# Kernel optimization log

Measured on AMD Instinct MI355X. Metric: run time of the kernel, lower is better.

## Reference

```python
import jax, jax.numpy as jnp
import numpy as np

VOCAB = 50000; T = 4096; EMBED = 500; H = 500  # hidden per direction (HIDDEN_SIZE=1000, bidirectional)
NUM_TAGS = 16; START = 14; STOP = 15
NEG = -10000.0


def setup_inputs() -> dict:
    key = jax.random.key(0)
    ks = jax.random.split(key, 16)
    n = lambda k, s, sc=0.1: (jax.random.normal(k, s) * sc).astype(jnp.float32)
    trans = n(ks[12], (NUM_TAGS, NUM_TAGS), 1.0)
    trans = trans.at[START, :].set(NEG).at[:, STOP].set(NEG)  # as in __init__
    return {
        "sent": jax.random.randint(ks[0], (T,), 0, VOCAB),
        "embed_w": n(ks[1], (VOCAB, EMBED), 1.0),
        "wih0": n(ks[2], (2, 4 * H, EMBED)),
        "whh0": n(ks[3], (2, 4 * H, H)),
        "bih0": n(ks[4], (2, 4 * H)),
        "bhh0": n(ks[5], (2, 4 * H)),
        "wih1": n(ks[6], (2, 4 * H, 2 * H)),
        "whh1": n(ks[7], (2, 4 * H, H)),
        "bih1": n(ks[8], (2, 4 * H)),
        "bhh1": n(ks[9], (2, 4 * H)),
        "w_out": n(ks[10], (NUM_TAGS, 2 * H)),
        "b_out": n(ks[11], (NUM_TAGS,)),
        "trans": trans,
        "h0": n(ks[13], (4, H), 1.0),  # init_hidden() uses randn; layout [layer*2+dir, H]
        "c0": n(ks[14], (4, H), 1.0),
    }


def _lstm_dir(x, wih, whh, bih, bhh, h0, c0):
    b = bih + bhh
    def cell(carry, xt):
        h, c = carry
        g = xt @ wih.T + h @ whh.T + b          # [4H], torch gate order i,f,g,o
        i, f, gg, o = jnp.split(g, 4)
        c = jax.nn.sigmoid(f) * c + jax.nn.sigmoid(i) * jnp.tanh(gg)
        h = jax.nn.sigmoid(o) * jnp.tanh(c)
        return (h, c), h
    _, hs = jax.lax.scan(cell, (h0, c0), x)
    return hs  # [T, H]


def _bilstm_layer(x, wih, whh, bih, bhh, h0, c0):
    fwd = _lstm_dir(x, wih[0], whh[0], bih[0], bhh[0], h0[0], c0[0])
    bwd = _lstm_dir(x[::-1], wih[1], whh[1], bih[1], bhh[1], h0[1], c0[1])[::-1]
    return jnp.concatenate([fwd, bwd], axis=-1)  # [T, 2H]


def _features(sent, embed_w, wih0, whh0, bih0, bhh0, wih1, whh1, bih1, bhh1, w_out, b_out, h0, c0):
    x = embed_w[sent]                                            # [T, EMBED]
    x = _bilstm_layer(x, wih0, whh0, bih0, bhh0, h0[0:2], c0[0:2])
    x = _bilstm_layer(x, wih1, whh1, bih1, bhh1, h0[2:4], c0[2:4])
    return x @ w_out.T + b_out                                   # [T, NUM_TAGS]


def _viterbi(feats, trans):
    score0 = jnp.full((NUM_TAGS,), NEG, dtype=feats.dtype).at[START].set(0.0)
    def step(score, feat):
        m = score[None, :] + trans               # m[tag, prev] = score[prev] + trans[tag, prev]
        return jnp.max(m, axis=1) + feat, jnp.argmax(m, axis=1)
    score, bptr = jax.lax.scan(step, score0, feats)              # bptr: [T, NUM_TAGS]
    score = score + trans[STOP]
    best_tag = jnp.argmax(score)
    best_score = score[best_tag]
    # faithful to the source backtrace: best_tag is NOT updated inside its loop,
    # so path = [bptr[1][bt], ..., bptr[T-1][bt], bt]
    path = jnp.concatenate([bptr[1:, best_tag], best_tag[None]])
    return best_score, path


def reference(sent, embed_w, wih0, whh0, bih0, bhh0, wih1, whh1, bih1, bhh1, w_out, b_out, trans, h0, c0):
    feats = _features(sent, embed_w, wih0, whh0, bih0, bhh0,
                      wih1, whh1, bih1, bhh1, w_out, b_out, h0, c0)
    return _viterbi(feats, trans)
```

## Files before the change

### kernel.cpp

```cpp
#include <hip/hip_runtime.h>


#define T_SEQ 4096
#define HPAD  512
#define NTAG  16


__global__ __launch_bounds__(256) void gin_gemm_k(
    const float* __restrict__ A, int KA,
    const int* __restrict__ sent, const float* __restrict__ embed_w,
    const float* __restrict__ wih, const float* __restrict__ bih,
    const float* __restrict__ bhh, int Kreal, float* __restrict__ G) {
  const int dir = blockIdx.z;
  const int bm = blockIdx.y, bn = blockIdx.x;
  const float* W = wih + (size_t)dir * 2000 * Kreal;

  __shared__ float As[2][16][128];
  __shared__ float Bs[2][16][128];
  __shared__ int   sSent[128];

  const int tid = threadIdx.x;
  const int tx = tid & 15, ty = tid >> 4;

  if (sent && tid < 128) sSent[tid] = sent[bm * 128 + tid];
  if (sent) __syncthreads();

  const int mA[2] = { (tid + 0) >> 2, (tid + 256) >> 2 };
  const int kA[2] = { ((tid + 0) & 3) * 4, ((tid + 256) & 3) * 4 };

  auto loadA = [&](int k0, int q) -> float4 {
    int m = mA[q], kc = kA[q];
    int k = k0 + kc;
    if (sent) {
      float4 z = {0.f, 0.f, 0.f, 0.f};
      if (k < 500)
        z = *reinterpret_cast<const float4*>(&embed_w[(size_t)sSent[m] * 500 + k]);
      return z;
    }
    return *reinterpret_cast<const float4*>(&A[(size_t)(bm * 128 + m) * KA + k]);
  };
  auto loadB = [&](int k0, int q) -> float4 {
    int n = mA[q], kc = kA[q];
    int nn = bn * 128 + n;
    int gate = nn >> 9, j = nn & 511;
    int k = k0 + kc;
    int jk = k & 511, half = k >> 9;
    float4 z = {0.f, 0.f, 0.f, 0.f};
    if (j < 500 && jk < 500)
      z = *reinterpret_cast<const float4*>(
          &W[(size_t)(gate * 500 + j) * Kreal + half * 500 + jk]);
    return z;
  };
  auto store = [&](int buf, int q, float4 av, float4 bv) {
    int m = mA[q], kc = kA[q];
    As[buf][kc + 0][m] = av.x; As[buf][kc + 1][m] = av.y;
    As[buf][kc + 2][m] = av.z; As[buf][kc + 3][m] = av.w;
    Bs[buf][kc + 0][m] = bv.x; Bs[buf][kc + 1][m] = bv.y;
    Bs[buf][kc + 2][m] = bv.z; Bs[buf][kc + 3][m] = bv.w;
  };

  {
    float4 a0 = loadA(0, 0), b0 = loadB(0, 0);
    float4 a1 = loadA(0, 1), b1 = loadB(0, 1);
    store(0, 0, a0, b0);
    store(0, 1, a1, b1);
  }
  __syncthreads();

  const int iters = KA >> 4;
  float acc[8][8] = {};

  for (int it = 0; it < iters; ++it) {
    const int cur = it & 1;
    const bool hasNext = (it + 1 < iters);
    float4 aP0, bP0, aP1, bP1;
    if (hasNext) {
      int k0n = (it + 1) << 4;
      aP0 = loadA(k0n, 0); bP0 = loadB(k0n, 0);
      aP1 = loadA(k0n, 1); bP1 = loadB(k0n, 1);
    }
#pragma unroll
    for (int kk = 0; kk < 16; kk++) {
      float a[8], b[8];
      *reinterpret_cast<float4*>(&a[0]) = *reinterpret_cast<const float4*>(&As[cur][kk][ty * 8]);
      *reinterpret_cast<float4*>(&a[4]) = *reinterpret_cast<const float4*>(&As[cur][kk][ty * 8 + 4]);
      *reinterpret_cast<float4*>(&b[0]) = *reinterpret_cast<const float4*>(&Bs[cur][kk][tx * 8]);
      *reinterpret_cast<float4*>(&b[4]) = *reinterpret_cast<const float4*>(&Bs[cur][kk][tx * 8 + 4]);
#pragma unroll
      for (int i = 0; i < 8; i++)
#pragma unroll
        for (int j = 0; j < 8; j++) acc[i][j] = fmaf(a[i], b[j], acc[i][j]);
    }
    if (hasNext) {
      store(cur ^ 1, 0, aP0, bP0);
      store(cur ^ 1, 1, aP1, bP1);
    }
    __syncthreads();
  }

#pragma unroll
  for (int i = 0; i < 8; i++) {
#pragma unroll
    for (int j = 0; j < 8; j++) {
      int m = bm * 128 + ty * 8 + i;
      int nn = bn * 128 + tx * 8 + j;
      int gate = nn >> 9, ju = nn & 511;
      float o = 0.0f;
      if (ju < 500) {
        int r = gate * 500 + ju;
        o = acc[i][j] + bih[dir * 2000 + r] + bhh[dir * 2000 + r];
      }
      G[((size_t)dir * T_SEQ + m) * 2048 + nn] = o;
    }
  }
}

__device__ __forceinline__ unsigned long long pack_hv(unsigned tag, float h) {
  return (unsigned long long)tag | ((unsigned long long)__float_as_uint(h) << 32);
}

__device__ __forceinline__ float fsig(float x) {
  float e = __expf(-x);
  return __builtin_amdgcn_rcpf(1.0f + e);
}
__device__ __forceinline__ float ftanhf(float x) {
  return fmaf(2.0f, fsig(x + x), -1.0f);
}

__global__ void hinit_k(const float* __restrict__ h0, int layer,
                        unsigned long long* __restrict__ hcomm) {
  int i = blockIdx.x * blockDim.x + threadIdx.x;
  int dir = i >> 10, par = (i >> 9) & 1, j = i & 511;
  unsigned long long v;
  if (par == 0) {
    float h = (j < 500) ? h0[(layer * 2 + dir) * 500 + j] : 0.0f;
    v = pack_hv(0u, h);
  } else {
    v = 0xFFFFFFFFull;
  }
  hcomm[(size_t)(dir * 2 + par) * HPAD + j] = v;
}

__global__ __launch_bounds__(1024)
__attribute__((amdgpu_waves_per_eu(4, 4)))
void lstm_k(
    const float* __restrict__ whh_base,
    const float* __restrict__ gin,
    const float* __restrict__ c0,
    float* __restrict__ xout,
    unsigned long long* __restrict__ hcomm,
    int layer) {
  __shared__ float part[16][68];
  __shared__ float hbuf[16][32];

  const int tid = threadIdx.x;
  const int dir = blockIdx.x >> 5;
  const int wgd = blockIdx.x & 31;
  const int w = tid >> 6;
  const int lane = tid & 63;

  const int gate = lane >> 4;
  const int ul   = lane & 15;
  const int j    = wgd * 16 + ul;
  const int row  = gate * 500 + j;

  float wreg[32];
  const float* Wd = whh_base + (size_t)dir * 2000 * 500;
#pragma unroll
  for (int i = 0; i < 32; i++) {
    int k = w * 32 + i;
    wreg[i] = (j < 500 && k < 500) ? Wd[(size_t)row * 500 + k] : 0.0f;
  }
#pragma unroll
  for (int i = 0; i < 32; i++) asm volatile("" : "+v"(wreg[i]));

  float c = 0.0f;
  if (w == 0 && lane < 16 && j < 500) c = c0[(layer * 2 + dir) * 500 + j];

  unsigned long long* hcd = hcomm + (size_t)dir * 2 * HPAD;
  bool dead = false;

  for (int t = 0; t < T_SEQ; t++) {
    const int t_in = (dir == 0) ? t : (T_SEQ - 1 - t);

    float gi = 0.0f;
    if (w == 0) {
      const float* gb = gin + ((size_t)dir * T_SEQ + t_in) * 2048;
      gi = gb[gate * 512 + j];
    }

    unsigned long long v = 0;
    if (!dead) {
      const unsigned long long* hp =
          hcd + (size_t)(t & 1) * HPAD + w * 32 + (lane & 31);
      int guard = 0;
      for (;;) {
        v = __hip_atomic_load(hp, __ATOMIC_RELAXED, __HIP_MEMORY_SCOPE_AGENT);
        if (__all((int)((unsigned)v == (unsigned)t))) break;
        if (++guard > (1 << 22)) { dead = true; break; }
      }
    }
    float hval = __uint_as_float((unsigned)(v >> 32));

    if (lane < 32) hbuf[w][lane] = hval;
    float a = 0.0f;
#pragma unroll
    for (int b = 0; b < 8; b++) {
      float4 hv = *reinterpret_cast<const float4*>(&hbuf[w][b * 4]);
      a = fmaf(wreg[b * 4 + 0], hv.x, a);
      a = fmaf(wreg[b * 4 + 1], hv.y, a);
      a = fmaf(wreg[b * 4 + 2], hv.z, a);
      a = fmaf(wreg[b * 4 + 3], hv.w, a);
    }
    part[w][lane] = a;
    __syncthreads();

    if (w == 0) {
      __builtin_amdgcn_s_setprio(1);
      float p0 = part[0][lane] + part[1][lane];
      float p1 = part[2][lane] + part[3][lane];
      float p2 = part[4][lane] + part[5][lane];
      float p3 = part[6][lane] + part[7][lane];
      float p4 = part[8][lane] + part[9][lane];
      float p5 = part[10][lane] + part[11][lane];
      float p6 = part[12][lane] + part[13][lane];
      float p7 = part[14][lane] + part[15][lane];
      float q0 = p0 + p1, q1 = p2 + p3, q2 = p4 + p5, q3 = p6 + p7;
      float s = gi + ((q0 + q1) + (q2 + q3));
      float nl = (gate == 2) ? ftanhf(s) : fsig(s);
      float xf = __shfl(nl, lane + 16, 64);
      float xg = __shfl(nl, lane + 32, 64);
      float xo = __shfl(nl, lane + 48, 64);
      if (lane < 16) {
        c = xf * c + nl * xg;
        float h = xo * ftanhf(c);
        __hip_atomic_store(hcd + (size_t)((t + 1) & 1) * HPAD + j,
                           pack_hv((unsigned)(t + 1), h),
                           __ATOMIC_RELAXED, __HIP_MEMORY_SCOPE_AGENT);
        if (j < 500)
          xout[(size_t)t_in * 1024 + (size_t)dir * HPAD + j] = h;
      }
      __builtin_amdgcn_s_setprio(0);
    }
  }
}

__global__ __launch_bounds__(256) void feats_k(
    const float* __restrict__ x2, const float* __restrict__ w_out,
    const float* __restrict__ b_out, float* __restrict__ feats) {
  int tid = threadIdx.x;
  int tag = tid & 15, tl = tid >> 4;
  int t = blockIdx.x * 16 + tl;
  float a0 = 0.0f, a1 = 0.0f, a2 = 0.0f, a3 = 0.0f;
  for (int k = 0; k < 1024; k += 4) {
    int jk = k & 511;
    const float* xr = x2 + (size_t)t * 1024 + k;
    const float* wr = w_out + tag * 1000 + (k >> 9) * 500 + jk;
    if (jk + 3 < 500) {
      a0 = fmaf(xr[0], wr[0], a0);
      a1 = fmaf(xr[1], wr[1], a1);
      a2 = fmaf(xr[2], wr[2], a2);
      a3 = fmaf(xr[3], wr[3], a3);
    } else if (jk < 500) {
#pragma unroll
      for (int e = 0; e < 4; e++)
        if (jk + e < 500) a0 = fmaf(xr[e], wr[e], a0);
    }
  }
  feats[t * 16 + tag] = ((a0 + a1) + (a2 + a3)) + b_out[tag];
}

__global__ __launch_bounds__(64) void viterbi_k(
    const float* __restrict__ feats, const float* __restrict__ trans,
    int* __restrict__ bptr, float* __restrict__ out) {
  int tid = threadIdx.x;
  int tag = tid & 15, pg = tid >> 4;
  float tr0 = trans[tag * 16 + pg * 4 + 0];
  float tr1 = trans[tag * 16 + pg * 4 + 1];
  float tr2 = trans[tag * 16 + pg * 4 + 2];
  float tr3 = trans[tag * 16 + pg * 4 + 3];
  float s = (tag == 14) ? 0.0f : -10000.0f;
  float ft = feats[tag];
  for (int t = 0; t < T_SEQ; t++) {
    float ftn = (t + 1 < T_SEQ) ? feats[(t + 1) * 16 + tag] : 0.0f;
    float c0 = __shfl(s, pg * 4 + 0, 64) + tr0;
    float c1 = __shfl(s, pg * 4 + 1, 64) + tr1;
    float c2 = __shfl(s, pg * 4 + 2, 64) + tr2;
    float c3 = __shfl(s, pg * 4 + 3, 64) + tr3;
    float bv = c0; int bi = pg * 4;
    if (c1 > bv) { bv = c1; bi = pg * 4 + 1; }
    if (c2 > bv) { bv = c2; bi = pg * 4 + 2; }
    if (c3 > bv) { bv = c3; bi = pg * 4 + 3; }
    float ov = __shfl_xor(bv, 16, 64); int oi = __shfl_xor(bi, 16, 64);
    if (ov > bv || (ov == bv && oi < bi)) { bv = ov; bi = oi; }
    ov = __shfl_xor(bv, 32, 64); oi = __shfl_xor(bi, 32, 64);
    if (ov > bv || (ov == bv && oi < bi)) { bv = ov; bi = oi; }
    s = bv + ft;
    ft = ftn;
    if (pg == 0) bptr[t * 16 + tag] = bi;
  }
  s += trans[15 * 16 + tag];
  float bv = s; int bi = tag;
  for (int mask = 1; mask < 16; mask <<= 1) {
    float ov = __shfl_xor(bv, mask, 16); int oi = __shfl_xor(bi, mask, 16);
    if (ov > bv || (ov == bv && oi < bi)) { bv = ov; bi = oi; }
  }
  if (tid == 0) out[0] = bv;
  int bt = bi;
  for (int i = tid; i < T_SEQ - 1; i += 64)
    out[1 + i] = (float)bptr[(i + 1) * 16 + bt];
  if (tid == 0) out[T_SEQ] = (float)bt;
}

extern "C" void kernel_launch(void* const* d_in, const int* in_sizes, int n_in,
                              void* d_out, int out_size, void* d_ws, size_t ws_size,
                              hipStream_t stream) {
  const int*   sent  = (const int*)d_in[0];
  const float* embed = (const float*)d_in[1];
  const float* wih0  = (const float*)d_in[2];
  const float* whh0  = (const float*)d_in[3];
  const float* bih0  = (const float*)d_in[4];
  const float* bhh0  = (const float*)d_in[5];
  const float* wih1  = (const float*)d_in[6];
  const float* whh1  = (const float*)d_in[7];
  const float* bih1  = (const float*)d_in[8];
  const float* bhh1  = (const float*)d_in[9];
  const float* w_out = (const float*)d_in[10];
  const float* b_out = (const float*)d_in[11];
  const float* trans = (const float*)d_in[12];
  const float* h0    = (const float*)d_in[13];
  const float* c0    = (const float*)d_in[14];
  float* out = (float*)d_out;

  char* ws = (char*)d_ws;
  float* x1    = (float*)(ws + 8388608);
  float* x2    = (float*)(ws + 25165824);
  float* gin   = (float*)(ws + 41943040);
  float* feats = (float*)(ws + 109051904);
  int*   bptr  = (int*)(ws + 109314048);
  unsigned long long* hcomm = (unsigned long long*)(ws + 109576192);

  gin_gemm_k<<<dim3(16, 32, 2), 256, 0, stream>>>(nullptr, 512, sent, embed,
                                                  wih0, bih0, bhh0, 500, gin);
  hinit_k<<<2, 1024, 0, stream>>>(h0, 0, hcomm);
  lstm_k<<<64, 1024, 0, stream>>>(whh0, gin, c0, x1, hcomm, 0);

  gin_gemm_k<<<dim3(16, 32, 2), 256, 0, stream>>>(x1, 1024, nullptr, nullptr,
                                                  wih1, bih1, bhh1, 1000, gin);
  hinit_k<<<2, 1024, 0, stream>>>(h0, 1, hcomm);
  lstm_k<<<64, 1024, 0, stream>>>(whh1, gin, c0, x2, hcomm, 1);

  feats_k<<<T_SEQ / 16, 256, 0, stream>>>(x2, w_out, b_out, feats);
  viterbi_k<<<1, 64, 0, stream>>>(feats, trans, bptr, out);
}
```

Before: 13.16 ms.

## Overlap layer-1 input GEMM with layer-0 recurrence via persistent progress queue

Fuses the layer-0 LSTM recurrence and the layer-1 input-projection GEMM into one persistent kernel. Extra workgroups take GEMM tiles from an atomic ticket counter and spin on per-workgroup progress flags until both directions have produced the required rows of x1. Tiles are ordered from the middle of the sequence outward, where forward and backward outputs become complete first. This hides most of the second GEMM behind the serial recurrence. The cost is contention from the GEMM workgroups for CU resources and memory bandwidth, which could slow the latency-critical recurrence, and reliance on cross-workgroup spin-waits.

Result: slower. 23.94 ms (+81.9%).

```diff
diff --git a/kernel.cpp b/kernel.cpp
--- a/kernel.cpp
+++ b/kernel.cpp
@@ -128,8 +128,11 @@
 }
 
 __global__ void hinit_k(const float* __restrict__ h0, int layer,
-                        unsigned long long* __restrict__ hcomm) {
+                        unsigned long long* __restrict__ hcomm,
+                        int* __restrict__ progq) {
   int i = blockIdx.x * blockDim.x + threadIdx.x;
+  if (i < 64) progq[i] = -1;
+  if (i == 64) progq[64] = 0;
   int dir = i >> 10, par = (i >> 9) & 1, j = i & 511;
   unsigned long long v;
   if (par == 0) {
@@ -143,13 +146,207 @@
 
 __global__ __launch_bounds__(1024)
 __attribute__((amdgpu_waves_per_eu(4, 4)))
-void lstm_k(
+void lstm_gemm_k(
     const float* __restrict__ whh_base,
     const float* __restrict__ gin,
     const float* __restrict__ c0,
     float* __restrict__ xout,
     unsigned long long* __restrict__ hcomm,
-    int layer) {
+    int* __restrict__ progq,
+    const float* __restrict__ wih1,
+    const float* __restrict__ bih1, const float* __restrict__ bhh1) {
+  __shared__ float part[16][68];
+  __shared__ float hbuf[16][32];
+  __shared__ float wAs[16][256];
+  __shared__ float wBs[16][128];
+  __shared__ int sTicket;
+
+  const int tid = threadIdx.x;
+  float* ginw = (float*)gin;
+
+  if (blockIdx.x < 64) {
+    const int dir = blockIdx.x >> 5;
+    const int wgd = blockIdx.x & 31;
+    const int w = tid >> 6;
+    const int lane = tid & 63;
+
+    const int gate = lane >> 4;
+    const int ul   = lane & 15;
+    const int j    = wgd * 16 + ul;
+    const int row  = gate * 500 + j;
+
+    float wreg[32];
+    const float* Wd = whh_base + (size_t)dir * 2000 * 500;
+#pragma unroll
+    for (int i = 0; i < 32; i++) {
+      int k = w * 32 + i;
+      wreg[i] = (j < 500 && k < 500) ? Wd[(size_t)row * 500 + k] : 0.0f;
+    }
+#pragma unroll
+    for (int i = 0; i < 32; i++) asm volatile("" : "+v"(wreg[i]));
+
+    float c = 0.0f;
+    if (w == 0 && lane < 16 && j < 500) c = c0[(0 * 2 + dir) * 500 + j];
+
+    unsigned long long* hcd = hcomm + (size_t)dir * 2 * HPAD;
+    bool dead = false;
+
+    for (int t = 0; t < T_SEQ; t++) {
+      const int t_in = (dir == 0) ? t : (T_SEQ - 1 - t);
+
+      float gi = 0.0f;
+      if (w == 0) {
+        const float* gb = gin + ((size_t)dir * T_SEQ + t_in) * 2048;
+        gi = gb[gate * 512 + j];
+      }
+
+      unsigned long long v = 0;
+      if (!dead) {
+        const unsigned long long* hp =
+            hcd + (size_t)(t & 1) * HPAD + w * 32 + (lane & 31);
+        int guard = 0;
+        for (;;) {
+          v = __hip_atomic_load(hp, __ATOMIC_RELAXED, __HIP_MEMORY_SCOPE_AGENT);
+          if (__all((int)((unsigned)v == (unsigned)t))) break;
+          if (++guard > (1 << 22)) { dead = true; break; }
+        }
+      }
+      float hval = __uint_as_float((unsigned)(v >> 32));
+
+      if (lane < 32) hbuf[w][lane] = hval;
+      float a = 0.0f;
+#pragma unroll
+      for (int b = 0; b < 8; b++) {
+        float4 hv = *reinterpret_cast<const float4*>(&hbuf[w][b * 4]);
+        a = fmaf(wreg[b * 4 + 0], hv.x, a);
+        a = fmaf(wreg[b * 4 + 1], hv.y, a);
+        a = fmaf(wreg[b * 4 + 2], hv.z, a);
+        a = fmaf(wreg[b * 4 + 3], hv.w, a);
+      }
+      part[w][lane] = a;
+      __syncthreads();
+
+      if (w == 0) {
+        __builtin_amdgcn_s_setprio(1);
+        float p0 = part[0][lane] + part[1][lane];
+        float p1 = part[2][lane] + part[3][lane];
+        float p2 = part[4][lane] + part[5][lane];
+        float p3 = part[6][lane] + part[7][lane];
+        float p4 = part[8][lane] + part[9][lane];
+        float p5 = part[10][lane] + part[11][lane];
+        float p6 = part[12][lane] + part[13][lane];
+        float p7 = part[14][lane] + part[15][lane];
+        float q0 = p0 + p1, q1 = p2 + p3, q2 = p4 + p5, q3 = p6 + p7;
+        float s = gi + ((q0 + q1) + (q2 + q3));
+        float nl = (gate == 2) ? ftanhf(s) : fsig(s);
+        float xf = __shfl(nl, lane + 16, 64);
+        float xg = __shfl(nl, lane + 32, 64);
+        float xo = __shfl(nl, lane + 48, 64);
+        if (lane < 16) {
+          c = xf * c + nl * xg;
+          float h = xo * ftanhf(c);
+          __hip_atomic_store(hcd + (size_t)((t + 1) & 1) * HPAD + j,
+                             pack_hv((unsigned)(t + 1), h),
+                             __ATOMIC_RELAXED, __HIP_MEMORY_SCOPE_AGENT);
+          if (j < 500)
+            xout[(size_t)t_in * 1024 + (size_t)dir * HPAD + j] = h;
+          if (lane == 0 && (t & 31) == 31)
+            __hip_atomic_store(&progq[dir * 32 + wgd], t,
+                               __ATOMIC_RELEASE, __HIP_MEMORY_SCOPE_AGENT);
+        }
+        __builtin_amdgcn_s_setprio(0);
+      }
+    }
+    return;
+  }
+
+  const int ty = tid >> 4, tx = tid & 15;
+  for (;;) {
+    if (tid == 0) sTicket = atomicAdd(&progq[64], 1);
+    __syncthreads();
+    int q = sTicket;
+    __syncthreads();
+    if (q >= 512) break;
+    int r = q >> 5;
+    int bm = (r & 1) ? 8 + (r >> 1) : 7 - (r >> 1);
+    int dir = (q >> 4) & 1;
+    int bn = q & 15;
+    int R0 = bm * 256;
+
+    if (tid < 64) {
+      int thr = (tid < 32) ? (R0 + 255) : (4095 - R0);
+      const int* pp = progq + tid;
+      int guard = 0;
+      for (;;) {
+        int pv = __hip_atomic_load(pp, __ATOMIC_ACQUIRE, __HIP_MEMORY_SCOPE_AGENT);
+        if (__all(pv >= thr)) break;
+        __builtin_amdgcn_s_sleep(8);
+        if (++guard > (1 << 24)) break;
+      }
+    }
+    __syncthreads();
+
+    const float* W = wih1 + (size_t)dir * 2000 * 1000;
+    float acc[4][8] = {};
+    for (int k0 = 0; k0 < 1024; k0 += 16) {
+      {
+        int m = tid >> 2, kc = (tid & 3) * 4;
+        float4 av = *reinterpret_cast<const float4*>(
+            &xout[(size_t)(R0 + m) * 1024 + k0 + kc]);
+        wAs[kc + 0][m] = av.x; wAs[kc + 1][m] = av.y;
+        wAs[kc + 2][m] = av.z; wAs[kc + 3][m] = av.w;
+      }
+      if (tid < 512) {
+        int n = tid >> 2, kc = (tid & 3) * 4;
+        int nn = bn * 128 + n;
+        int gate = nn >> 9, j = nn & 511;
+        int k = k0 + kc;
+        int jk = k & 511, half = k >> 9;
+        float4 bv = {0.f, 0.f, 0.f, 0.f};
+        if (j < 500 && jk < 500)
+          bv = *reinterpret_cast<const float4*>(
+              &W[(size_t)(gate * 500 + j) * 1000 + half * 500 + jk]);
+        wBs[kc + 0][n] = bv.x; wBs[kc + 1][n] = bv.y;
+        wBs[kc + 2][n] = bv.z; wBs[kc + 3][n] = bv.w;
+      }
+      __syncthreads();
+#pragma unroll
+      for (int kk = 0; kk < 16; kk++) {
+        float a[4], b[8];
+        *reinterpret_cast<float4*>(&a[0]) = *reinterpret_cast<const float4*>(&wAs[kk][ty * 4]);
+        *reinterpret_cast<float4*>(&b[0]) = *reinterpret_cast<const float4*>(&wBs[kk][tx * 8]);
+        *reinterpret_cast<float4*>(&b[4]) = *reinterpret_cast<const float4*>(&wBs[kk][tx * 8 + 4]);
+#pragma unroll
+        for (int i = 0; i < 4; i++)
+#pragma unroll
+          for (int jj = 0; jj < 8; jj++) acc[i][jj] = fmaf(a[i], b[jj], acc[i][jj]);
+      }
+      __syncthreads();
+    }
+#pragma unroll
+    for (int i = 0; i < 4; i++) {
+#pragma unroll
+      for (int jj = 0; jj < 8; jj++) {
+        int t = R0 + ty * 4 + i;
+        int nn = bn * 128 + tx * 8 + jj;
+        int gate = nn >> 9, ju = nn & 511;
+        float o = 0.0f;
+        if (ju < 500) {
+          int rr = gate * 500 + ju;
+          o = acc[i][jj] + bih1[dir * 2000 + rr] + bhh1[dir * 2000 + rr];
+        }
+        ginw[((size_t)dir * T_SEQ + t) * 2048 + nn] = o;
+      }
+    }
+  }
+}
+
+__global__ __launch_bounds__(1024)
+__attribute__((amdgpu_waves_per_eu(4, 4)))
+void lstm_k(
+    const float* __restrict__ whh_base, const float* __restrict__ gin,
+    const float* __restrict__ c0, float* __restrict__ xout,
+    unsigned long long* __restrict__ hcomm, int layer) {
   __shared__ float part[16][68];
   __shared__ float hbuf[16][32];
 
@@ -333,6 +530,7 @@
   float* out = (float*)d_out;
 
   char* ws = (char*)d_ws;
+  int*   progq = (int*)(ws + 0);
   float* x1    = (float*)(ws + 8388608);
   float* x2    = (float*)(ws + 25165824);
   float* gin   = (float*)(ws + 41943040);
@@ -342,12 +540,11 @@
 
   gin_gemm_k<<<dim3(16, 32, 2), 256, 0, stream>>>(nullptr, 512, sent, embed,
                                                   wih0, bih0, bhh0, 500, gin);
-  hinit_k<<<2, 1024, 0, stream>>>(h0, 0, hcomm);
-  lstm_k<<<64, 1024, 0, stream>>>(whh0, gin, c0, x1, hcomm, 0);
-
-  gin_gemm_k<<<dim3(16, 32, 2), 256, 0, stream>>>(x1, 1024, nullptr, nullptr,
-                                                  wih1, bih1, bhh1, 1000, gin);
-  hinit_k<<<2, 1024, 0, stream>>>(h0, 1, hcomm);
+  hinit_k<<<2, 1024, 0, stream>>>(h0, 0, hcomm, progq);
+  lstm_gemm_k<<<256, 1024, 0, stream>>>(whh0, gin, c0, x1, hcomm, progq,
+                                        wih1, bih1, bhh1);
+
+  hinit_k<<<2, 1024, 0, stream>>>(h0, 1, hcomm, progq);
   lstm_k<<<64, 1024, 0, stream>>>(whh1, gin, c0, x2, hcomm, 1);
 
   feats_k<<<T_SEQ / 16, 256, 0, stream>>>(x2, w_out, b_out, feats);
```
